# Kernel tuning notes

Measured on AMD Instinct MI355X. Metric: run time of the kernel, lower is better.

The kernel has to match this reference:

```python
import jax, jax.numpy as jnp
import numpy as np

Q = 3
PAD = 4
STRIDE = 1
DIL = 1
MAX_SHIFT = 4.0


def setup_inputs() -> dict:
    key = jax.random.key(0)
    k1, k2, k3, k4 = jax.random.split(key, 4)
    B, Cin, L, Cout, K = 16, 128, 8192, 128, 9
    x = jax.random.normal(k1, (B, Cin, L), jnp.float32)
    # shifts stored pre-divided by max_shift (as in reset_parameters); y-shift zeroed
    sx = jax.random.uniform(k2, (Cin, 1), jnp.float32, minval=-0.5, maxval=0.5)
    shifts = jnp.concatenate([sx, jnp.zeros((Cin, 1), jnp.float32)], axis=1)
    weights = jax.random.normal(k3, (Cout, Q * Cin, K), jnp.float32) * 0.02
    bias = jax.random.normal(k4, (Cout,), jnp.float32) * 0.01
    return {"x": x, "weights": weights, "bias": bias, "shifts": shifts}


def _channel_shift(x, shift):
    # x: [B, C, L]; shift: [C]. Equivalent to affine_grid+grid_sample with H=1,
    # align_corners=False, zeros padding: output[i] = lerp(x, i + shift).
    B, C, L = x.shape
    pos = jnp.arange(L, dtype=x.dtype)[None, :] + shift[:, None]  # [C, L]
    i0 = jnp.floor(pos).astype(jnp.int32)
    i1 = i0 + 1
    w1 = (pos - i0.astype(x.dtype))[None]  # [1, C, L]

    def gather(idx):
        valid = ((idx >= 0) & (idx < L)).astype(x.dtype)[None]  # zeros padding
        idx_b = jnp.broadcast_to(jnp.clip(idx, 0, L - 1)[None], x.shape)
        return jnp.take_along_axis(x, idx_b, axis=2) * valid

    return gather(i0) * (1.0 - w1) + gather(i1) * w1


def reference(x, weights, bias, shifts):
    xs = _channel_shift(x, shifts[:, 0] * MAX_SHIFT)  # [B, C, L]
    # q-order power expansion along channels: [x, x^2, ..., x^q]
    xq = jnp.concatenate([xs ** i for i in range(1, Q + 1)], axis=1)  # [B, q*C, L]
    out = jax.lax.conv_general_dilated(
        xq, weights,
        window_strides=(STRIDE,), padding=[(PAD, PAD)],
        rhs_dilation=(DIL,), dimension_numbers=("NCH", "OIH", "NCH"))
    return out + bias[None, :, None]
```

## Files before the change

### kernel.cpp

```cpp
#include <hip/hip_runtime.h>


#define B_    16
#define CIN   128
#define L_    8192
#define COUT  128
#define K_    9
#define QMAX  3
#define KQ    (QMAX * CIN)
#define KTOT  (K_ * KQ)
#define BK    64
#define GUARD 4
#define LROWS (L_ + 2 * GUARD)
#define XQOFF (1u << 20)
#define XSTR  73

typedef __attribute__((ext_vector_type(8)))  short bf16x8;
typedef __attribute__((ext_vector_type(16))) float f32x16;
typedef __attribute__((ext_vector_type(4)))  int   int4v;

__device__ __forceinline__ unsigned short f2bf(float v) {
    union { float f; unsigned u; } cv; cv.f = v;
    unsigned u = cv.u;
    return (unsigned short)((u + 0x7FFFu + ((u >> 16) & 1u)) >> 16);
}

__global__ __launch_bounds__(256) void prep_weights(
    const float* __restrict__ w, unsigned short* __restrict__ wa)
{
    int g = blockIdx.x * 256 + threadIdx.x;
    if (g >= COUT * KTOT) return;
    const int c   = g >> 13;
    const int r   = g & 8191;
    const int co  = r >> 6;
    const int s8  = (r >> 3) & 7;
    const int i   = r & 7;
    const int kk  = ((s8 ^ (co & 7)) << 3) | i;
    const int k   = c * BK + kk;
    const int tap = k / KQ;
    const int qc  = k - tap * KQ;
    wa[g] = f2bf(w[((size_t)co * KQ + qc) * K_ + tap]);
}

__global__ __launch_bounds__(256) void xq_prep(
    const float* __restrict__ x, const float* __restrict__ shifts,
    unsigned short* __restrict__ xq)
{
    __shared__ float xtile[128 * XSTR];
    const int l0   = blockIdx.x * 64;
    const int b    = blockIdx.y;
    const int tid  = threadIdx.x;
    const int lane = tid & 63;
    const int w4   = tid >> 6;
    const float* xb = x + (size_t)b * CIN * L_;

    float rv[32], rn[4];
    const int gcol = l0 - 4 + lane;
    const bool cok = (gcol >= 0) & (gcol < L_);
#pragma unroll
    for (int j = 0; j < 32; ++j) {
        const int r = w4 * 32 + j;
        rv[j] = cok ? xb[(size_t)r * L_ + gcol] : 0.0f;
    }
    const int ncol = l0 + 60 + (tid & 7);
    const bool nok = ncol < L_;
#pragma unroll
    for (int it = 0; it < 4; ++it) {
        const int r = it * 32 + (tid >> 3);
        rn[it] = nok ? xb[(size_t)r * L_ + ncol] : 0.0f;
    }
#pragma unroll
    for (int j = 0; j < 32; ++j)
        xtile[(w4 * 32 + j) * XSTR + lane] = rv[j];
#pragma unroll
    for (int it = 0; it < 4; ++it)
        xtile[(it * 32 + (tid >> 3)) * XSTR + 64 + (tid & 7)] = rn[it];
    __syncthreads();

    {
        const int ci    = tid & 127;
        const int lhalf = tid >> 7;
        const float sh = shifts[2 * ci] * 4.0f;
        const float fl = floorf(sh);
        const int  ifl = (int)fl;
        const float w1 = sh - fl;
        int c0 = lhalf * 32 + 4 + ifl;
        unsigned short* orow =
            xq + ((size_t)b * LROWS + l0 + GUARD + lhalf * 32) * KQ + ci;
        float v_prev = xtile[ci * XSTR + c0];
#pragma unroll
        for (int j = 0; j < 32; ++j) {
            const float v_next = xtile[ci * XSTR + c0 + 1];
            const float xs = fmaf(w1, v_next - v_prev, v_prev);
            const float x2 = xs * xs;
            const float x3 = x2 * xs;
            orow[0]   = f2bf(xs);
            orow[128] = f2bf(x2);
            orow[256] = f2bf(x3);
            v_prev = v_next;
            ++c0;
            orow += KQ;
        }
    }

    if (blockIdx.x == 0) {
        int4v* g0 = (int4v*)(xq + (size_t)b * LROWS * KQ);
        if (tid < 192) g0[tid] = (int4v){0, 0, 0, 0};
    }
    if (blockIdx.x == gridDim.x - 1) {
        int4v* g1 = (int4v*)(xq + ((size_t)b * LROWS + L_ + GUARD) * KQ);
        if (tid < 192) g1[tid] = (int4v){0, 0, 0, 0};
    }
}

__global__ __launch_bounds__(256, 4) void gemm(
    const unsigned short* __restrict__ wa,
    const unsigned short* __restrict__ xq,
    const float*          __restrict__ bias,
    float*                __restrict__ out)
{
    __shared__ __align__(16) unsigned short ldsA[COUT * BK];
    __shared__ __align__(16) unsigned short ldsB[136 * BK];

    const int l0   = blockIdx.x * 128;
    const int b    = blockIdx.y;
    const int tid  = threadIdx.x;
    const int lane = tid & 63;
    const int w    = tid >> 6;
    const int cobase = (w >> 1) * 64;
    const int nbase  = (w & 1) * 64;
    const int n5 = lane & 31;
    const int h  = lane >> 5;

    const int bj_row = lane >> 3;
    const size_t bLaneOff = (size_t)bj_row * KQ + (size_t)(((lane & 7) ^ (bj_row & 7)) << 3);

    int aaddr[2][4];
#pragma unroll
    for (int fi = 0; fi < 2; ++fi)
#pragma unroll
        for (int kc = 0; kc < 4; ++kc) {
            const int ar = cobase + fi * 32 + n5;
            aaddr[fi][kc] = ar * 128 + ((((kc << 1) | h) ^ (ar & 7)) << 4);
        }

    f32x16 acc[2][2];
#pragma unroll
    for (int i = 0; i < 2; ++i)
#pragma unroll
        for (int j = 0; j < 2; ++j) acc[i][j] = (f32x16){};

    const unsigned short* xqb   = xq + (size_t)b * LROWS * KQ;
    const unsigned short* bbase = xqb + (size_t)l0 * KQ + bLaneOff;

#pragma unroll 1
    for (int s = 0; s < 6; ++s) {
        const unsigned short* bsrc = bbase + s * 64;
#pragma unroll
        for (int i = 0; i < 4; ++i) {
            const int g = w * 4 + i;
            __builtin_amdgcn_global_load_lds(
                (const __attribute__((address_space(1))) void*)(bsrc + (size_t)g * 8 * KQ),
                (__attribute__((address_space(3))) void*)((char*)ldsB + g * 1024),
                16, 0, 0);
        }
        if (w == 0)
            __builtin_amdgcn_global_load_lds(
                (const __attribute__((address_space(1))) void*)(bsrc + (size_t)16 * 8 * KQ),
                (__attribute__((address_space(3))) void*)((char*)ldsB + 16 * 1024),
                16, 0, 0);

#pragma unroll 1
        for (int tap = 0; tap < K_; ++tap) {
            const int c = tap * 6 + s;
            const unsigned short* agsrc = wa + (size_t)c * 8192 + (size_t)(w * 4) * 512 + lane * 8;
#pragma unroll
            for (int i = 0; i < 4; ++i)
                __builtin_amdgcn_global_load_lds(
                    (const __attribute__((address_space(1))) void*)(agsrc + i * 512),
                    (__attribute__((address_space(3))) void*)((char*)ldsA + (w * 4 + i) * 1024),
                    16, 0, 0);
            __syncthreads();
#pragma unroll
            for (int kc = 0; kc < 4; ++kc) {
                const int br0 = tap + nbase + n5;
                const int ba0 = br0 * 128 + ((((kc << 1) | h) ^ (br0 & 7)) << 4);
                const int ba1 = ba0 + 32 * 128;
                const bf16x8 a0 = *(const bf16x8*)((const char*)ldsA + aaddr[0][kc]);
                const bf16x8 a1 = *(const bf16x8*)((const char*)ldsA + aaddr[1][kc]);
                const bf16x8 b0 = *(const bf16x8*)((const char*)ldsB + ba0);
                const bf16x8 b1 = *(const bf16x8*)((const char*)ldsB + ba1);
                acc[0][0] = __builtin_amdgcn_mfma_f32_32x32x16_bf16(a0, b0, acc[0][0], 0, 0, 0);
                acc[0][1] = __builtin_amdgcn_mfma_f32_32x32x16_bf16(a0, b1, acc[0][1], 0, 0, 0);
                acc[1][0] = __builtin_amdgcn_mfma_f32_32x32x16_bf16(a1, b0, acc[1][0], 0, 0, 0);
                acc[1][1] = __builtin_amdgcn_mfma_f32_32x32x16_bf16(a1, b1, acc[1][1], 0, 0, 0);
            }
            __syncthreads();
        }
    }

#pragma unroll
    for (int fi = 0; fi < 2; ++fi)
#pragma unroll
        for (int bj = 0; bj < 2; ++bj)
#pragma unroll
            for (int r = 0; r < 16; ++r) {
                const int co = cobase + fi * 32 + (r & 3) + 8 * (r >> 2) + 4 * h;
                const int l  = l0 + nbase + bj * 32 + n5;
                out[((size_t)(b * COUT + co)) * L_ + l] = acc[fi][bj][r] + bias[co];
            }
}

extern "C" void kernel_launch(void* const* d_in, const int* in_sizes, int n_in,
                              void* d_out, int out_size, void* d_ws, size_t ws_size,
                              hipStream_t stream) {
    const float* x      = (const float*)d_in[0];
    const float* w      = (const float*)d_in[1];
    const float* bias   = (const float*)d_in[2];
    const float* shifts = (const float*)d_in[3];
    float* out = (float*)d_out;

    const size_t need = (size_t)XQOFF + (size_t)B_ * LROWS * KQ * 2;
    if (ws_size < need) return;

    unsigned short* wa = (unsigned short*)d_ws;
    unsigned short* xq = (unsigned short*)((char*)d_ws + XQOFF);

    const int nw = COUT * KTOT;
    prep_weights<<<(nw + 255) / 256, 256, 0, stream>>>(w, wa);

    dim3 gq(L_ / 64, B_);
    xq_prep<<<gq, 256, 0, stream>>>(x, shifts, xq);

    dim3 gg(L_ / 128, B_);
    gemm<<<gg, 256, 0, stream>>>(wa, xq, bias, out);
}
```

Baseline: 241.1 us.

## Load weight fragments directly from global into registers, drop A LDS staging

Weights are prepacked into a fragment-major layout so each lane loads its MFMA A operands straight from global memory (L2) into registers. The LDS tile for A is removed, and the per-tap __syncthreads pair becomes one barrier per B stage. The intent is to cut LDS traffic and barrier stalls, at the cost of more global/L2 load latency exposed per tap with no prefetching, plus duplicate weight loads across the two waves sharing a cobase.

```diff
diff --git a/kernel.cpp b/kernel.cpp
--- a/kernel.cpp
+++ b/kernel.cpp
@@ -30,15 +30,18 @@
 {
     int g = blockIdx.x * 256 + threadIdx.x;
     if (g >= COUT * KTOT) return;
-    const int c   = g >> 13;
-    const int r   = g & 8191;
-    const int co  = r >> 6;
-    const int s8  = (r >> 3) & 7;
-    const int i   = r & 7;
-    const int kk  = ((s8 ^ (co & 7)) << 3) | i;
-    const int k   = c * BK + kk;
-    const int tap = k / KQ;
-    const int qc  = k - tap * KQ;
+    const int blk    = g >> 9;
+    const int within = g & 511;
+    const int lane   = within >> 3;
+    const int i      = within & 7;
+    const int kc     = blk & 3;
+    const int fi     = (blk >> 2) & 1;
+    const int f      = (blk >> 3) & 1;
+    const int c      = blk >> 4;
+    const int co     = f * 64 + fi * 32 + (lane & 31);
+    const int k      = c * 64 + kc * 16 + (lane >> 5) * 8 + i;
+    const int tap    = k / KQ;
+    const int qc     = k - tap * KQ;
     wa[g] = f2bf(w[((size_t)co * KQ + qc) * K_ + tap]);
 }
 
@@ -119,7 +122,6 @@
     const float*          __restrict__ bias,
     float*                __restrict__ out)
 {
-    __shared__ __align__(16) unsigned short ldsA[COUT * BK];
     __shared__ __align__(16) unsigned short ldsB[136 * BK];
 
     const int l0   = blockIdx.x * 128;
@@ -127,7 +129,8 @@
     const int tid  = threadIdx.x;
     const int lane = tid & 63;
     const int w    = tid >> 6;
-    const int cobase = (w >> 1) * 64;
+    const int f      = w >> 1;
+    const int cobase = f * 64;
     const int nbase  = (w & 1) * 64;
     const int n5 = lane & 31;
     const int h  = lane >> 5;
@@ -135,15 +138,6 @@
     const int bj_row = lane >> 3;
     const size_t bLaneOff = (size_t)bj_row * KQ + (size_t)(((lane & 7) ^ (bj_row & 7)) << 3);
 
-    int aaddr[2][4];
-#pragma unroll
-    for (int fi = 0; fi < 2; ++fi)
-#pragma unroll
-        for (int kc = 0; kc < 4; ++kc) {
-            const int ar = cobase + fi * 32 + n5;
-            aaddr[fi][kc] = ar * 128 + ((((kc << 1) | h) ^ (ar & 7)) << 4);
-        }
-
     f32x16 acc[2][2];
 #pragma unroll
     for (int i = 0; i < 2; ++i)
@@ -152,6 +146,7 @@
 
     const unsigned short* xqb   = xq + (size_t)b * LROWS * KQ;
     const unsigned short* bbase = xqb + (size_t)l0 * KQ + bLaneOff;
+    const unsigned short* abase = wa + ((size_t)f << 12) + (size_t)lane * 8;
 
 #pragma unroll 1
     for (int s = 0; s < 6; ++s) {
@@ -169,34 +164,32 @@
                 (const __attribute__((address_space(1))) void*)(bsrc + (size_t)16 * 8 * KQ),
                 (__attribute__((address_space(3))) void*)((char*)ldsB + 16 * 1024),
                 16, 0, 0);
+        __syncthreads();
 
 #pragma unroll 1
         for (int tap = 0; tap < K_; ++tap) {
             const int c = tap * 6 + s;
-            const unsigned short* agsrc = wa + (size_t)c * 8192 + (size_t)(w * 4) * 512 + lane * 8;
-#pragma unroll
-            for (int i = 0; i < 4; ++i)
-                __builtin_amdgcn_global_load_lds(
-                    (const __attribute__((address_space(1))) void*)(agsrc + i * 512),
-                    (__attribute__((address_space(3))) void*)((char*)ldsA + (w * 4 + i) * 1024),
-                    16, 0, 0);
-            __syncthreads();
+            const unsigned short* ab = abase + ((size_t)c << 13);
+            bf16x8 A[2][4];
+#pragma unroll
+            for (int fi = 0; fi < 2; ++fi)
+#pragma unroll
+                for (int kc = 0; kc < 4; ++kc)
+                    A[fi][kc] = *(const bf16x8*)(ab + (size_t)((fi << 2) | kc) * 512);
 #pragma unroll
             for (int kc = 0; kc < 4; ++kc) {
                 const int br0 = tap + nbase + n5;
                 const int ba0 = br0 * 128 + ((((kc << 1) | h) ^ (br0 & 7)) << 4);
                 const int ba1 = ba0 + 32 * 128;
-                const bf16x8 a0 = *(const bf16x8*)((const char*)ldsA + aaddr[0][kc]);
-                const bf16x8 a1 = *(const bf16x8*)((const char*)ldsA + aaddr[1][kc]);
                 const bf16x8 b0 = *(const bf16x8*)((const char*)ldsB + ba0);
                 const bf16x8 b1 = *(const bf16x8*)((const char*)ldsB + ba1);
-                acc[0][0] = __builtin_amdgcn_mfma_f32_32x32x16_bf16(a0, b0, acc[0][0], 0, 0, 0);
-                acc[0][1] = __builtin_amdgcn_mfma_f32_32x32x16_bf16(a0, b1, acc[0][1], 0, 0, 0);
-                acc[1][0] = __builtin_amdgcn_mfma_f32_32x32x16_bf16(a1, b0, acc[1][0], 0, 0, 0);
-                acc[1][1] = __builtin_amdgcn_mfma_f32_32x32x16_bf16(a1, b1, acc[1][1], 0, 0, 0);
+                acc[0][0] = __builtin_amdgcn_mfma_f32_32x32x16_bf16(A[0][kc], b0, acc[0][0], 0, 0, 0);
+                acc[0][1] = __builtin_amdgcn_mfma_f32_32x32x16_bf16(A[0][kc], b1, acc[0][1], 0, 0, 0);
+                acc[1][0] = __builtin_amdgcn_mfma_f32_32x32x16_bf16(A[1][kc], b0, acc[1][0], 0, 0, 0);
+                acc[1][1] = __builtin_amdgcn_mfma_f32_32x32x16_bf16(A[1][kc], b1, acc[1][1], 0, 0, 0);
             }
-            __syncthreads();
         }
+        __syncthreads();
     }
 
 #pragma unroll
```

After: 253.6 us. 1.05x slower.

## Double-buffer weight tiles and widen GEMM tile to 256 columns

Applied to the files above, without the earlier changes.

The GEMM now covers 256 output positions per block instead of 128, so each weight tile fetched into LDS feeds twice as many MFMAs. It also double-buffers the weight tile, issuing the next tap's load before computing the current one, using explicit vmcnt waits, raw barriers and a raised wave priority. The intent is to hide global-to-LDS latency and cut weight traffic per output. The cost is more accumulator registers, occupancy lowered to 2 blocks, and half as many blocks in the grid.

```diff
diff --git a/kernel.cpp b/kernel.cpp
--- a/kernel.cpp
+++ b/kernel.cpp
@@ -14,6 +14,7 @@
 #define LROWS (L_ + 2 * GUARD)
 #define XQOFF (1u << 20)
 #define XSTR  73
+#define BROWS 264
 
 typedef __attribute__((ext_vector_type(8)))  short bf16x8;
 typedef __attribute__((ext_vector_type(16))) float f32x16;
@@ -113,22 +114,22 @@
     }
 }
 
-__global__ __launch_bounds__(256, 4) void gemm(
+__global__ __launch_bounds__(256, 2) void gemm(
     const unsigned short* __restrict__ wa,
     const unsigned short* __restrict__ xq,
     const float*          __restrict__ bias,
     float*                __restrict__ out)
 {
-    __shared__ __align__(16) unsigned short ldsA[COUT * BK];
-    __shared__ __align__(16) unsigned short ldsB[136 * BK];
-
-    const int l0   = blockIdx.x * 128;
+    __shared__ __align__(16) unsigned short ldsA[2][COUT * BK];
+    __shared__ __align__(16) unsigned short ldsB[BROWS * BK];
+
+    const int l0   = blockIdx.x * 256;
     const int b    = blockIdx.y;
     const int tid  = threadIdx.x;
     const int lane = tid & 63;
     const int w    = tid >> 6;
     const int cobase = (w >> 1) * 64;
-    const int nbase  = (w & 1) * 64;
+    const int nbase  = (w & 1) * 128;
     const int n5 = lane & 31;
     const int h  = lane >> 5;
 
@@ -144,57 +145,90 @@
             aaddr[fi][kc] = ar * 128 + ((((kc << 1) | h) ^ (ar & 7)) << 4);
         }
 
-    f32x16 acc[2][2];
+    f32x16 acc[2][4];
 #pragma unroll
     for (int i = 0; i < 2; ++i)
 #pragma unroll
-        for (int j = 0; j < 2; ++j) acc[i][j] = (f32x16){};
+        for (int j = 0; j < 4; ++j) acc[i][j] = (f32x16){};
 
     const unsigned short* xqb   = xq + (size_t)b * LROWS * KQ;
     const unsigned short* bbase = xqb + (size_t)l0 * KQ + bLaneOff;
-
+    const unsigned short* aw    = wa + (size_t)(w * 4) * 512 + (size_t)lane * 8;
+
+#define STAGE_B(sv)                                                            \
+    {                                                                          \
+        const unsigned short* bsrc = bbase + (sv) * 64;                        \
+        _Pragma("unroll")                                                      \
+        for (int i = 0; i < 8; ++i) {                                          \
+            const int g = w * 8 + i;                                           \
+            __builtin_amdgcn_global_load_lds(                                  \
+                (const __attribute__((address_space(1))) void*)(bsrc + (size_t)g * 8 * KQ), \
+                (__attribute__((address_space(3))) void*)((char*)ldsB + g * 1024), \
+                16, 0, 0);                                                     \
+        }                                                                      \
+        if (w == 0)                                                            \
+            __builtin_amdgcn_global_load_lds(                                  \
+                (const __attribute__((address_space(1))) void*)(bsrc + (size_t)32 * 8 * KQ), \
+                (__attribute__((address_space(3))) void*)((char*)ldsB + 32 * 1024), \
+                16, 0, 0);                                                     \
+    }
+
+#define LOAD_A(cv, buf)                                                        \
+    {                                                                          \
+        const unsigned short* agsrc = aw + (size_t)(cv) * 8192;                \
+        char* adst = (char*)ldsA[buf];                                         \
+        _Pragma("unroll")                                                      \
+        for (int i = 0; i < 4; ++i)                                            \
+            __builtin_amdgcn_global_load_lds(                                  \
+                (const __attribute__((address_space(1))) void*)(agsrc + i * 512), \
+                (__attribute__((address_space(3))) void*)(adst + (w * 4 + i) * 1024), \
+                16, 0, 0);                                                     \
+    }
+
+    STAGE_B(0);
+    LOAD_A(0, 0);
+    __syncthreads();
+
+    int par = 0;
 #pragma unroll 1
     for (int s = 0; s < 6; ++s) {
-        const unsigned short* bsrc = bbase + s * 64;
-#pragma unroll
-        for (int i = 0; i < 4; ++i) {
-            const int g = w * 4 + i;
-            __builtin_amdgcn_global_load_lds(
-                (const __attribute__((address_space(1))) void*)(bsrc + (size_t)g * 8 * KQ),
-                (__attribute__((address_space(3))) void*)((char*)ldsB + g * 1024),
-                16, 0, 0);
-        }
-        if (w == 0)
-            __builtin_amdgcn_global_load_lds(
-                (const __attribute__((address_space(1))) void*)(bsrc + (size_t)16 * 8 * KQ),
-                (__attribute__((address_space(3))) void*)((char*)ldsB + 16 * 1024),
-                16, 0, 0);
-
 #pragma unroll 1
         for (int tap = 0; tap < K_; ++tap) {
-            const int c = tap * 6 + s;
-            const unsigned short* agsrc = wa + (size_t)c * 8192 + (size_t)(w * 4) * 512 + lane * 8;
-#pragma unroll
-            for (int i = 0; i < 4; ++i)
-                __builtin_amdgcn_global_load_lds(
-                    (const __attribute__((address_space(1))) void*)(agsrc + i * 512),
-                    (__attribute__((address_space(3))) void*)((char*)ldsA + (w * 4 + i) * 1024),
-                    16, 0, 0);
-            __syncthreads();
+            if (tap < 8) {
+                LOAD_A((tap + 1) * 6 + s, par ^ 1);
+                asm volatile("s_waitcnt vmcnt(4)" ::: "memory");
+            } else if (s < 5) {
+                LOAD_A(s + 1, par ^ 1);
+                asm volatile("s_waitcnt vmcnt(4)" ::: "memory");
+            } else {
+                asm volatile("s_waitcnt vmcnt(0)" ::: "memory");
+            }
+            __builtin_amdgcn_s_barrier();
+            __builtin_amdgcn_sched_barrier(0);
+
+            __builtin_amdgcn_s_setprio(1);
+            const char* Ab = (const char*)ldsA[par];
 #pragma unroll
             for (int kc = 0; kc < 4; ++kc) {
                 const int br0 = tap + nbase + n5;
                 const int ba0 = br0 * 128 + ((((kc << 1) | h) ^ (br0 & 7)) << 4);
-                const int ba1 = ba0 + 32 * 128;
-                const bf16x8 a0 = *(const bf16x8*)((const char*)ldsA + aaddr[0][kc]);
-                const bf16x8 a1 = *(const bf16x8*)((const char*)ldsA + aaddr[1][kc]);
-                const bf16x8 b0 = *(const bf16x8*)((const char*)ldsB + ba0);
-                const bf16x8 b1 = *(const bf16x8*)((const char*)ldsB + ba1);
-                acc[0][0] = __builtin_amdgcn_mfma_f32_32x32x16_bf16(a0, b0, acc[0][0], 0, 0, 0);
-                acc[0][1] = __builtin_amdgcn_mfma_f32_32x32x16_bf16(a0, b1, acc[0][1], 0, 0, 0);
-                acc[1][0] = __builtin_amdgcn_mfma_f32_32x32x16_bf16(a1, b0, acc[1][0], 0, 0, 0);
-                acc[1][1] = __builtin_amdgcn_mfma_f32_32x32x16_bf16(a1, b1, acc[1][1], 0, 0, 0);
+                const bf16x8 a0 = *(const bf16x8*)(Ab + aaddr[0][kc]);
+                const bf16x8 a1 = *(const bf16x8*)(Ab + aaddr[1][kc]);
+#pragma unroll
+                for (int bj = 0; bj < 4; ++bj) {
+                    const bf16x8 bb = *(const bf16x8*)((const char*)ldsB + ba0 + bj * 4096);
+                    acc[0][bj] = __builtin_amdgcn_mfma_f32_32x32x16_bf16(a0, bb, acc[0][bj], 0, 0, 0);
+                    acc[1][bj] = __builtin_amdgcn_mfma_f32_32x32x16_bf16(a1, bb, acc[1][bj], 0, 0, 0);
+                }
             }
+            __builtin_amdgcn_s_setprio(0);
+            __builtin_amdgcn_sched_barrier(0);
+            __builtin_amdgcn_s_barrier();
+            __builtin_amdgcn_sched_barrier(0);
+            par ^= 1;
+        }
+        if (s < 5) {
+            STAGE_B(s + 1);
             __syncthreads();
         }
     }
@@ -202,13 +236,15 @@
 #pragma unroll
     for (int fi = 0; fi < 2; ++fi)
 #pragma unroll
-        for (int bj = 0; bj < 2; ++bj)
+        for (int bj = 0; bj < 4; ++bj)
 #pragma unroll
             for (int r = 0; r < 16; ++r) {
                 const int co = cobase + fi * 32 + (r & 3) + 8 * (r >> 2) + 4 * h;
                 const int l  = l0 + nbase + bj * 32 + n5;
                 out[((size_t)(b * COUT + co)) * L_ + l] = acc[fi][bj][r] + bias[co];
             }
+#undef STAGE_B
+#undef LOAD_A
 }
 
 extern "C" void kernel_launch(void* const* d_in, const int* in_sizes, int n_in,
@@ -232,6 +268,6 @@
     dim3 gq(L_ / 64, B_);
     xq_prep<<<gq, 256, 0, stream>>>(x, shifts, xq);
 
-    dim3 gg(L_ / 128, B_);
+    dim3 gg(L_ / 256, B_);
     gemm<<<gg, 256, 0, stream>>>(wa, xq, bias, out);
 }
```

New measurement: 239.3 us. No clear change (-0.7%).
